# Kernel optimization log

Hardware: AMD Instinct MI355X
Metric: run time of the kernel (lower is better)

## Reference

```python
import jax, jax.numpy as jnp
import numpy as np


def _conv3x3(x, w, b):
    # NCHW conv, stride 1, pad 1
    y = jax.lax.conv_general_dilated(x, w, (1, 1), ((1, 1), (1, 1)),
                                     dimension_numbers=('NCHW', 'OIHW', 'NCHW'))
    return y + b[None, :, None, None]


def _deform_conv3x3(x, offset, w):
    # Deformable conv v1: 3x3, stride 1, pad 1, 1 deformable group, no bias.
    # offset: [B, 18, H, W] laid out as (dy_k, dx_k) for k = 0..8 (row-major taps).
    B, C, H, W = x.shape
    K = 9
    off = offset.reshape(B, K, 2, H, W)
    ky, kx = jnp.meshgrid(jnp.arange(3), jnp.arange(3), indexing='ij')
    ky = (ky.reshape(K) - 1).astype(x.dtype)  # kernel tap y-offset, pad=1
    kx = (kx.reshape(K) - 1).astype(x.dtype)
    hh = jnp.arange(H, dtype=x.dtype)
    ww = jnp.arange(W, dtype=x.dtype)
    # sampling locations [B, K, H, W]
    sy = hh[None, None, :, None] + ky[None, :, None, None] + off[:, :, 0]
    sx = ww[None, None, None, :] + kx[None, :, None, None] + off[:, :, 1]
    y0 = jnp.floor(sy)
    x0 = jnp.floor(sx)
    ly = sy - y0  # fractional parts
    lx = sx - x0
    x_flat = x.reshape(B, C, H * W)

    def gather(yi, xi, wgt):
        # zero-padding semantics: corners outside the image contribute 0
        valid = (yi >= 0) & (yi < H) & (xi >= 0) & (xi < W)
        idx = (jnp.clip(yi, 0, H - 1).astype(jnp.int32) * W
               + jnp.clip(xi, 0, W - 1).astype(jnp.int32)).reshape(B, 1, K * H * W)
        v = jnp.take_along_axis(x_flat, idx, axis=2).reshape(B, C, K, H, W)
        return v * (wgt * valid.astype(x.dtype))[:, None]

    sampled = (gather(y0,     x0,     (1 - ly) * (1 - lx))
             + gather(y0,     x0 + 1, (1 - ly) * lx)
             + gather(y0 + 1, x0,     ly * (1 - lx))
             + gather(y0 + 1, x0 + 1, ly * lx))  # [B, C, K, H, W]
    return jnp.einsum('bckhw,ock->bohw', sampled, w.reshape(w.shape[0], C, K))


def setup_inputs() -> dict:
    key = jax.random.key(0)
    ks = jax.random.split(key, 8)
    C, O = 256, 256
    return {
        'kernel': jax.random.normal(ks[0], (16, C, 16, 16), jnp.float32),
        'search': jax.random.normal(ks[1], (16, C, 32, 32), jnp.float32),
        'Toffset_w': jax.random.normal(ks[2], (18, C, 3, 3), jnp.float32) * 0.02,
        'Toffset_b': jnp.zeros((18,), jnp.float32),
        'Tdeform_w': jax.random.normal(ks[3], (O, C, 3, 3), jnp.float32) * 0.02,
        'Soffset_w': jax.random.normal(ks[4], (18, C, 3, 3), jnp.float32) * 0.02,
        'Soffset_b': jnp.zeros((18,), jnp.float32),
        'Sdeform_w': jax.random.normal(ks[5], (O, C, 3, 3), jnp.float32) * 0.02,
    }


def reference(kernel, search, Toffset_w, Toffset_b, Tdeform_w,
              Soffset_w, Soffset_b, Sdeform_w):
    kernel_offset = _conv3x3(kernel, Toffset_w, Toffset_b)
    kernel_out = _deform_conv3x3(kernel, kernel_offset, Tdeform_w)
    search_offset = _conv3x3(search, Soffset_w, Soffset_b)
    search_out = _deform_conv3x3(search, search_offset, Sdeform_w)
    return (kernel_out, search_out, kernel_offset, search_offset)
```

## Files before the change

### kernel.cpp

```cpp
#include <hip/hip_runtime.h>

#define CIN   256
#define OC    256
#define K_TOT 2304
#define CCH   32
#define NCHK  8
#define KCH   288
#define SSTR  296
#define DM    64
#define DUNITS (DM * 9 * 4)

#define N_DW  (OC * K_TOT)
#define N_OW  (32 * K_TOT)
#define N_CVT (2 * N_DW + 2 * N_OW)
#define CVT_BLOCKS (N_CVT / 4 / 256)

typedef short  bf16x8 __attribute__((ext_vector_type(8)));
typedef float  f32x4  __attribute__((ext_vector_type(4)));
typedef unsigned short ushort_t;

__device__ __forceinline__ ushort_t f2bf(float f) {
    unsigned u = __builtin_bit_cast(unsigned, f);
    u += 0x7fffu + ((u >> 16) & 1u);
    return (ushort_t)(u >> 16);
}
__device__ __forceinline__ float bf2f(short s) {
    return __builtin_bit_cast(float, ((unsigned)(unsigned short)s) << 16);
}

__global__ __launch_bounds__(256) void prep_k(
    const float* __restrict__ tdw, const float* __restrict__ sdw,
    const float* __restrict__ tow, const float* __restrict__ sow,
    const float* __restrict__ kin, const float* __restrict__ sin_,
    ushort_t* __restrict__ wk_d, ushort_t* __restrict__ ws_d,
    ushort_t* __restrict__ wk_o, ushort_t* __restrict__ ws_o,
    ushort_t* __restrict__ xt_k, ushort_t* __restrict__ xt_s)
{
    __shared__ ushort_t tile[64][264];

    if (blockIdx.x < CVT_BLOCKS) {
        const int i = (blockIdx.x * 256 + threadIdx.x) * 4;
        const float* src; ushort_t* dst; int j; bool offw = false;
        if (i < N_DW)                    { src = tdw; dst = wk_d; j = i; }
        else if (i < 2 * N_DW)           { src = sdw; dst = ws_d; j = i - N_DW; }
        else if (i < 2 * N_DW + N_OW)    { src = tow; dst = wk_o; j = i - 2 * N_DW; offw = true; }
        else                             { src = sow; dst = ws_o; j = i - 2 * N_DW - N_OW; offw = true; }
        const int oc = j / K_TOT;
        const int k  = j - oc * K_TOT;
        const int cc = k / KCH;
        const int r  = k - cc * KCH;
        const int tap = r >> 5;
        const int cl  = r & 31;
        ushort4 o4 = {0, 0, 0, 0};
        if (!offw || oc < 18) {
            const float* sp = &src[((size_t)oc * CIN + cc * 32 + cl) * 9 + tap];
            o4.x = f2bf(sp[0]); o4.y = f2bf(sp[9]); o4.z = f2bf(sp[18]); o4.w = f2bf(sp[27]);
        }
        *(ushort4*)&dst[j] = o4;
        return;
    }

    const int bx2 = blockIdx.x - CVT_BLOCKS;
    int H, W, b, px0; const float* x; ushort_t* xt;
    if (bx2 < 64) {
        H = 16; W = 16; x = kin; xt = xt_k;
        b = bx2 >> 2; px0 = (bx2 & 3) * 64;
    } else {
        int t2 = bx2 - 64;
        H = 32; W = 32; x = sin_; xt = xt_s;
        b = t2 >> 4; px0 = (t2 & 15) * 64;
    }
    const int HW = H * W;
    const int t = threadIdx.x, lane = t & 63, wv = t >> 6;
    const float* xb = x + (size_t)b * CIN * HW;

    for (int it = 0; it < 16; ++it) {
        const int ch = wv * 64 + it * 4 + (lane >> 4);
        const int pq = (lane & 15) * 4;
        float4 v = *(const float4*)&xb[(size_t)ch * HW + px0 + pq];
        tile[pq + 0][ch] = f2bf(v.x);
        tile[pq + 1][ch] = f2bf(v.y);
        tile[pq + 2][ch] = f2bf(v.z);
        tile[pq + 3][ch] = f2bf(v.w);
    }
    __syncthreads();
    for (int it = 0; it < 8; ++it) {
        const int px = it * 8 + wv * 2 + (lane >> 5);
        const int cg = (lane & 31) * 8;
        bf16x8 v = *(const bf16x8*)&tile[px][cg];
        *(bf16x8*)&xt[((size_t)b * HW + px0 + px) * 256 + cg] = v;
    }
}

__global__ __launch_bounds__(256, 2) void conv_gemm_k(
    const ushort_t* __restrict__ xt_k, const ushort_t* __restrict__ kwgt,
    const float* __restrict__ kbias, float* __restrict__ kout,
    const ushort_t* __restrict__ xt_s, const ushort_t* __restrict__ swgt,
    const float* __restrict__ sbias, float* __restrict__ sout)
{
    __shared__ float sred[3][4][2][64][4];

    int H, W, sh, b, px0;
    const ushort_t* xt; const ushort_t* wgt; const float* bias; float* out;
    if (blockIdx.x < 64) {
        H = 16; W = 16; sh = 4; xt = xt_k; wgt = kwgt; bias = kbias; out = kout;
        b = blockIdx.x >> 2; px0 = (blockIdx.x & 3) * 64;
    } else {
        int t2 = blockIdx.x - 64;
        H = 32; W = 32; sh = 5; xt = xt_s; wgt = swgt; bias = sbias; out = sout;
        b = t2 >> 4; px0 = (t2 & 15) * 64;
    }
    const int HW = H * W;
    const int t = threadIdx.x, lane = t & 63, kh = t >> 6;
    const int l15 = lane & 15;
    const int cg8 = (lane >> 4) * 8;
    const ushort_t* xtb = xt + (size_t)b * HW * 256;

    int h[4], wc[4];
#pragma unroll
    for (int mt = 0; mt < 4; ++mt) {
        const int px = px0 + mt * 16 + l15;
        h[mt]  = px >> sh;
        wc[mt] = px & (W - 1);
    }
    const ushort_t* wrow0 = wgt + (size_t)(l15)      * K_TOT + cg8;
    const ushort_t* wrow1 = wgt + (size_t)(16 + l15) * K_TOT + cg8;

    f32x4 acc[4][2] = {};
    for (int cc = kh * 2; cc < kh * 2 + 2; ++cc) {
        const int cb = cc * 32 + cg8;
#pragma unroll
        for (int ks = 0; ks < 9; ++ks) {
            const bf16x8 b0 = *(const bf16x8*)&wrow0[(size_t)cc * KCH + ks * 32];
            const bf16x8 b1 = *(const bf16x8*)&wrow1[(size_t)cc * KCH + ks * 32];
            const int dy = ks / 3 - 1, dx = ks % 3 - 1;
#pragma unroll
            for (int mt = 0; mt < 4; ++mt) {
                const int y  = h[mt] + dy;
                const int xx = wc[mt] + dx;
                const bool ok = ((unsigned)y < (unsigned)H) && ((unsigned)xx < (unsigned)W);
                bf16x8 a = {};
                if (ok) a = *(const bf16x8*)&xtb[(size_t)(((y << sh) + xx) * 256 + cb)];
                acc[mt][0] = __builtin_amdgcn_mfma_f32_16x16x32_bf16(a, b0, acc[mt][0], 0, 0, 0);
                acc[mt][1] = __builtin_amdgcn_mfma_f32_16x16x32_bf16(a, b1, acc[mt][1], 0, 0, 0);
            }
        }
    }

    if (kh > 0) {
#pragma unroll
        for (int mt = 0; mt < 4; ++mt)
#pragma unroll
            for (int nt = 0; nt < 2; ++nt)
                *(float4*)&sred[kh - 1][mt][nt][lane][0] = *(float4*)&acc[mt][nt];
    }
    __syncthreads();
    if (kh == 0) {
        const int prow = (lane >> 4) * 4;
#pragma unroll
        for (int nt = 0; nt < 2; ++nt) {
            const int oc = nt * 16 + l15;
            if (oc < 18) {
                const float bs = bias[oc];
#pragma unroll
                for (int mt = 0; mt < 4; ++mt) {
                    float4 r = *(float4*)&acc[mt][nt];
#pragma unroll
                    for (int q = 0; q < 3; ++q) {
                        const float4 o = *(const float4*)&sred[q][mt][nt][lane][0];
                        r.x += o.x; r.y += o.y; r.z += o.z; r.w += o.w;
                    }
                    r.x += bs; r.y += bs; r.z += bs; r.w += bs;
                    *(float4*)(out + ((size_t)b * 18 + oc) * HW + px0 + mt * 16 + prow) = r;
                }
            }
        }
    }
}

__device__ __forceinline__ void dcn_load4(
    bf16x8* c, const ushort_t* __restrict__ xtb, int4 id, int cb)
{
    c[0] = *(const bf16x8*)&xtb[(size_t)id.x * 256 + cb];
    c[1] = *(const bf16x8*)&xtb[(size_t)id.y * 256 + cb];
    c[2] = *(const bf16x8*)&xtb[(size_t)id.z * 256 + cb];
    c[3] = *(const bf16x8*)&xtb[(size_t)id.w * 256 + cb];
}
__device__ __forceinline__ void dcn_proc2(
    ushort_t* swb, int so, const bf16x8* c, float4 wt)
{
    bf16x8 r;
#pragma unroll
    for (int j = 0; j < 8; ++j) {
        const float v = wt.x * bf2f(c[0][j]) + wt.y * bf2f(c[1][j])
                      + wt.z * bf2f(c[2][j]) + wt.w * bf2f(c[3][j]);
        r[j] = (short)f2bf(v);
    }
    *(bf16x8*)&swb[so] = r;
}

__global__ __launch_bounds__(512, 4) void deform_gemm_k(
    const ushort_t* __restrict__ xt_k, const float* __restrict__ koffs,
    const ushort_t* __restrict__ kwgt, float* __restrict__ kout,
    const ushort_t* __restrict__ xt_s, const float* __restrict__ soffs,
    const ushort_t* __restrict__ swgt_, float* __restrict__ sout)
{
    __shared__ __align__(16) ushort_t smp[DM][SSTR];
    __shared__ __align__(16) int      sidx[DM][9][4];
    __shared__ __align__(16) float    swt [DM][9][4];

    int H, W, b, px0;
    const ushort_t* xt; const float* offs; const ushort_t* wgt; float* out;
    if (blockIdx.x < 64) {
        H = 16; W = 16; xt = xt_k; offs = koffs; wgt = kwgt; out = kout;
        b = blockIdx.x >> 2; px0 = (blockIdx.x & 3) * 64;
    } else {
        int t2 = blockIdx.x - 64;
        H = 32; W = 32; xt = xt_s; offs = soffs; wgt = swgt_; out = sout;
        b = t2 >> 4; px0 = (t2 & 15) * 64;
    }
    const int HW = H * W;
    const int t = threadIdx.x, lane = t & 63, wv = t >> 6;

#pragma unroll
    for (int u = 0; u < 2; ++u) {
        const int s = t + u * 512;
        if (s < DM * 9) {
            const int p = s / 9, k = s - 9 * p;
            const int pix = px0 + p;
            const int h  = pix / W;
            const int wc = pix - h * W;
            const float* ob = offs + (size_t)b * 18 * HW;
            const float dy = ob[(2 * k    ) * HW + pix];
            const float dx = ob[(2 * k + 1) * HW + pix];
            const float sy = (float)(h  + k / 3 - 1) + dy;
            const float sx = (float)(wc + k % 3 - 1) + dx;
            const float y0f = floorf(sy), x0f = floorf(sx);
            const float ly = sy - y0f, lx = sx - x0f;
            const int y0 = (int)y0f, x0 = (int)x0f;
#pragma unroll
            for (int j = 0; j < 4; ++j) {
                const int yy = y0 + (j >> 1);
                const int xx = x0 + (j & 1);
                const bool ok = ((unsigned)yy < (unsigned)H) && ((unsigned)xx < (unsigned)W);
                sidx[p][k][j] = min(max(yy, 0), H - 1) * W + min(max(xx, 0), W - 1);
                const float wj = ((j >> 1) ? ly : 1.f - ly) * ((j & 1) ? lx : 1.f - lx);
                swt[p][k][j] = ok ? wj : 0.f;
            }
        }
    }
    __syncthreads();

    const ushort_t* xtb = xt + (size_t)b * HW * 256;
    const int l15 = lane & 15;
    const int cg8 = (lane >> 4) * 8;
    const int ocb = wv * 32;
    const bool live4 = (t < 256);

    const int g0  = t >> 2;
    const int cgE = (t & 3) * 8;
    int uso[5];
#pragma unroll
    for (int q = 0; q < 5; ++q) {
        const int g  = g0 + q * 128;
        const int px = g / 9, tap = g - 9 * px;
        uso[q] = px * SSTR + tap * 32 + (t & 3) * 8;
    }

    const ushort_t* wrow0 = wgt + (size_t)(ocb      + l15) * K_TOT + cg8;
    const ushort_t* wrow1 = wgt + (size_t)(ocb + 16 + l15) * K_TOT + cg8;
    ushort_t* smpb = &smp[0][0];
    const int4*   sidxF = (const int4*)  &sidx[0][0][0];
    const float4* swtF  = (const float4*)&swt [0][0][0];

    f32x4 acc[4][2] = {};

    for (int cc = 0; cc < NCHK; ++cc) {
        const int cb = cc * 32 + cgE;
        const size_t kg0 = (size_t)cc * KCH;

#pragma unroll
        for (int q = 0; q < 5; ++q) {
            if (q < 4 || live4) {
                const int  g  = g0 + q * 128;
                const int4   id = sidxF[g];
                const float4 wt = swtF[g];
                bf16x8 c[4];
                dcn_load4(c, xtb, id, cb);
                dcn_proc2(smpb, uso[q], c, wt);
            }
        }

        const bf16x8 pb0 = *(const bf16x8*)&wrow0[kg0];
        const bf16x8 pb1 = *(const bf16x8*)&wrow1[kg0];

        asm volatile("s_waitcnt lgkmcnt(0)" ::: "memory");
        __builtin_amdgcn_sched_barrier(0);
        __builtin_amdgcn_s_barrier();
        __builtin_amdgcn_sched_barrier(0);

        __builtin_amdgcn_s_setprio(1);
#pragma unroll
        for (int ks = 0; ks < 9; ++ks) {
            const bf16x8 b0 = (ks == 0) ? pb0 : *(const bf16x8*)&wrow0[kg0 + (size_t)ks * 32];
            const bf16x8 b1 = (ks == 0) ? pb1 : *(const bf16x8*)&wrow1[kg0 + (size_t)ks * 32];
            bf16x8 a[4];
#pragma unroll
            for (int mt = 0; mt < 4; ++mt)
                a[mt] = *(const bf16x8*)&smp[mt * 16 + l15][ks * 32 + cg8];
#pragma unroll
            for (int mt = 0; mt < 4; ++mt) {
                acc[mt][0] = __builtin_amdgcn_mfma_f32_16x16x32_bf16(a[mt], b0, acc[mt][0], 0, 0, 0);
                acc[mt][1] = __builtin_amdgcn_mfma_f32_16x16x32_bf16(a[mt], b1, acc[mt][1], 0, 0, 0);
            }
        }
        __builtin_amdgcn_s_setprio(0);

        if (cc < NCHK - 1) {
            __builtin_amdgcn_sched_barrier(0);
            __builtin_amdgcn_s_barrier();
            __builtin_amdgcn_sched_barrier(0);
        }
    }

    const int prow = (lane >> 4) * 4;
#pragma unroll
    for (int mt = 0; mt < 4; ++mt) {
#pragma unroll
        for (int nt = 0; nt < 2; ++nt) {
            const int oc = ocb + nt * 16 + l15;
            float* op = out + ((size_t)b * OC + oc) * HW + px0 + mt * 16 + prow;
            *(float4*)op = *(float4*)&acc[mt][nt];
        }
    }
}

extern "C" void kernel_launch(void* const* d_in, const int* in_sizes, int n_in,
                              void* d_out, int out_size, void* d_ws, size_t ws_size,
                              hipStream_t stream) {
    const float* kin = (const float*)d_in[0];
    const float* sin_ = (const float*)d_in[1];
    const float* tow = (const float*)d_in[2];
    const float* tob = (const float*)d_in[3];
    const float* tdw = (const float*)d_in[4];
    const float* sow = (const float*)d_in[5];
    const float* sob = (const float*)d_in[6];
    const float* sdw = (const float*)d_in[7];

    float* out = (float*)d_out;
    float* out_k  = out;
    float* out_s  = out_k + (size_t)16 * 256 * 16 * 16;
    float* out_ko = out_s + (size_t)16 * 256 * 32 * 32;
    float* out_so = out_ko + (size_t)16 * 18 * 16 * 16;

    ushort_t* wk_d = (ushort_t*)d_ws;
    ushort_t* ws_d = wk_d + N_DW;
    ushort_t* wk_o = ws_d + N_DW;
    ushort_t* ws_o = wk_o + N_OW;
    ushort_t* xt_k = ws_o + N_OW;
    ushort_t* xt_s = xt_k + (size_t)16 * 256 * 256;

    prep_k<<<dim3(CVT_BLOCKS + 320), 256, 0, stream>>>(
        tdw, sdw, tow, sow, kin, sin_,
        wk_d, ws_d, wk_o, ws_o, xt_k, xt_s);

    conv_gemm_k<<<dim3(320), 256, 0, stream>>>(
        xt_k, wk_o, tob, out_ko, xt_s, ws_o, sob, out_so);

    deform_gemm_k<<<dim3(320), 512, 0, stream>>>(
        xt_k, out_ko, wk_d, out_k, xt_s, out_so, ws_d, out_s);
}
```

Measured before the change: 207.7 us.

## Software-pipeline deformable gathers and weight loads, remap blocks across XCDs

Restructures the deform-GEMM main loop so bilinear corner gathers for several tap groups are issued before earlier groups are processed. The first group for the next channel chunk is prefetched before the MFMA phase, so gather latency overlaps the matrix math. Weight fragments are double-buffered across the ks loop, and block indices are remapped so consecutive blocks (which go to different XCDs) handle different batches. This adds register pressure from holding five gather sets, which could cut occupancy under the 512x4 launch bounds.

```diff
diff --git a/kernel.cpp b/kernel.cpp
--- a/kernel.cpp
+++ b/kernel.cpp
@@ -8,7 +8,6 @@
 #define KCH   288
 #define SSTR  296
 #define DM    64
-#define DUNITS (DM * 9 * 4)
 
 #define N_DW  (OC * K_TOT)
 #define N_OW  (32 * K_TOT)
@@ -212,12 +211,14 @@
     int H, W, b, px0;
     const ushort_t* xt; const float* offs; const ushort_t* wgt; float* out;
     if (blockIdx.x < 64) {
+        const int xcd = blockIdx.x & 7, i = blockIdx.x >> 3;
         H = 16; W = 16; xt = xt_k; offs = koffs; wgt = kwgt; out = kout;
-        b = blockIdx.x >> 2; px0 = (blockIdx.x & 3) * 64;
+        b = xcd + 8 * (i & 1); px0 = (i >> 1) * 64;
     } else {
-        int t2 = blockIdx.x - 64;
+        const int t2 = blockIdx.x - 64;
+        const int xcd = t2 & 7, i = t2 >> 3;
         H = 32; W = 32; xt = xt_s; offs = soffs; wgt = swgt_; out = sout;
-        b = t2 >> 4; px0 = (t2 & 15) * 64;
+        b = xcd + 8 * (i & 1); px0 = (i >> 1) * 64;
     }
     const int HW = H * W;
     const int t = threadIdx.x, lane = t & 63, wv = t >> 6;
@@ -274,25 +275,38 @@
     const float4* swtF  = (const float4*)&swt [0][0][0];
 
     f32x4 acc[4][2] = {};
+    bf16x8 c0[4], c1[4], c2[4], c3[4], c4[4];
+    float4 w0v, w1v, w2v, w3v, w4v = {};
+    bf16x8 bq[2][2];
+
+    {
+        const int4 id = sidxF[g0];
+        w0v = swtF[g0];
+        dcn_load4(c0, xtb, id, cgE);
+    }
 
     for (int cc = 0; cc < NCHK; ++cc) {
         const int cb = cc * 32 + cgE;
         const size_t kg0 = (size_t)cc * KCH;
 
-#pragma unroll
-        for (int q = 0; q < 5; ++q) {
-            if (q < 4 || live4) {
-                const int  g  = g0 + q * 128;
-                const int4   id = sidxF[g];
-                const float4 wt = swtF[g];
-                bf16x8 c[4];
-                dcn_load4(c, xtb, id, cb);
-                dcn_proc2(smpb, uso[q], c, wt);
-            }
-        }
-
-        const bf16x8 pb0 = *(const bf16x8*)&wrow0[kg0];
-        const bf16x8 pb1 = *(const bf16x8*)&wrow1[kg0];
+        { const int4 id = sidxF[g0 + 128]; w1v = swtF[g0 + 128]; dcn_load4(c1, xtb, id, cb); }
+        { const int4 id = sidxF[g0 + 256]; w2v = swtF[g0 + 256]; dcn_load4(c2, xtb, id, cb); }
+        bq[0][0] = *(const bf16x8*)&wrow0[kg0];
+        bq[0][1] = *(const bf16x8*)&wrow1[kg0];
+
+        dcn_proc2(smpb, uso[0], c0, w0v);
+        { const int4 id = sidxF[g0 + 384]; w3v = swtF[g0 + 384]; dcn_load4(c3, xtb, id, cb); }
+        dcn_proc2(smpb, uso[1], c1, w1v);
+        if (live4) { const int4 id = sidxF[g0 + 512]; w4v = swtF[g0 + 512]; dcn_load4(c4, xtb, id, cb); }
+        dcn_proc2(smpb, uso[2], c2, w2v);
+        dcn_proc2(smpb, uso[3], c3, w3v);
+        if (live4) dcn_proc2(smpb, uso[4], c4, w4v);
+
+        if (cc < NCHK - 1) {
+            const int4 id = sidxF[g0];
+            w0v = swtF[g0];
+            dcn_load4(c0, xtb, id, cb + 32);
+        }
 
         asm volatile("s_waitcnt lgkmcnt(0)" ::: "memory");
         __builtin_amdgcn_sched_barrier(0);
@@ -302,16 +316,18 @@
         __builtin_amdgcn_s_setprio(1);
 #pragma unroll
         for (int ks = 0; ks < 9; ++ks) {
-            const bf16x8 b0 = (ks == 0) ? pb0 : *(const bf16x8*)&wrow0[kg0 + (size_t)ks * 32];
-            const bf16x8 b1 = (ks == 0) ? pb1 : *(const bf16x8*)&wrow1[kg0 + (size_t)ks * 32];
+            if (ks < 8) {
+                bq[(ks + 1) & 1][0] = *(const bf16x8*)&wrow0[kg0 + (size_t)(ks + 1) * 32];
+                bq[(ks + 1) & 1][1] = *(const bf16x8*)&wrow1[kg0 + (size_t)(ks + 1) * 32];
+            }
             bf16x8 a[4];
 #pragma unroll
             for (int mt = 0; mt < 4; ++mt)
                 a[mt] = *(const bf16x8*)&smp[mt * 16 + l15][ks * 32 + cg8];
 #pragma unroll
             for (int mt = 0; mt < 4; ++mt) {
-                acc[mt][0] = __builtin_amdgcn_mfma_f32_16x16x32_bf16(a[mt], b0, acc[mt][0], 0, 0, 0);
-                acc[mt][1] = __builtin_amdgcn_mfma_f32_16x16x32_bf16(a[mt], b1, acc[mt][1], 0, 0, 0);
+                acc[mt][0] = __builtin_amdgcn_mfma_f32_16x16x32_bf16(a[mt], bq[ks & 1][0], acc[mt][0], 0, 0, 0);
+                acc[mt][1] = __builtin_amdgcn_mfma_f32_16x16x32_bf16(a[mt], bq[ks & 1][1], acc[mt][1], 0, 0, 0);
             }
         }
         __builtin_amdgcn_s_setprio(0);
```

After: 265.6 us. 1.28x slower.

## Warp-specialize deform GEMM into producer/consumer waves with double-buffered samples

Applied to the files above, without the earlier changes.

Splits the deformable-conv GEMM block into four producer waves that bilinearly sample into a double-buffered LDS tile and four consumer waves that run MFMA with register-prefetched, nontemporal weight loads. The pixel tile shrinks from 64 to 32, so twice as many blocks launch, and blocks are remapped so batches spread across XCDs. The goal is to overlap gather latency with matrix math and raise parallelism. In exchange, each block now reads the weights for half as many pixels, which doubles total weight traffic. Half the waves also do no MFMA work.

```diff
diff --git a/kernel.cpp b/kernel.cpp
--- a/kernel.cpp
+++ b/kernel.cpp
@@ -7,8 +7,7 @@
 #define NCHK  8
 #define KCH   288
 #define SSTR  296
-#define DM    64
-#define DUNITS (DM * 9 * 4)
+#define DM    32
 
 #define N_DW  (OC * K_TOT)
 #define N_OW  (32 * K_TOT)
@@ -26,6 +25,9 @@
 }
 __device__ __forceinline__ float bf2f(short s) {
     return __builtin_bit_cast(float, ((unsigned)(unsigned short)s) << 16);
+}
+__device__ __forceinline__ bf16x8 ldnt(const ushort_t* p) {
+    return __builtin_nontemporal_load((const bf16x8*)p);
 }
 
 __global__ __launch_bounds__(256) void prep_k(
@@ -205,48 +207,46 @@
     const ushort_t* __restrict__ xt_s, const float* __restrict__ soffs,
     const ushort_t* __restrict__ swgt_, float* __restrict__ sout)
 {
-    __shared__ __align__(16) ushort_t smp[DM][SSTR];
+    __shared__ __align__(16) ushort_t smp[2][DM][SSTR];
     __shared__ __align__(16) int      sidx[DM][9][4];
     __shared__ __align__(16) float    swt [DM][9][4];
 
     int H, W, b, px0;
     const ushort_t* xt; const float* offs; const ushort_t* wgt; float* out;
-    if (blockIdx.x < 64) {
+    if (blockIdx.x < 128) {
+        const int xcd = blockIdx.x & 7, i = blockIdx.x >> 3;
         H = 16; W = 16; xt = xt_k; offs = koffs; wgt = kwgt; out = kout;
-        b = blockIdx.x >> 2; px0 = (blockIdx.x & 3) * 64;
+        b = xcd + 8 * (i & 1); px0 = (i >> 1) * 32;
     } else {
-        int t2 = blockIdx.x - 64;
+        const int t2 = blockIdx.x - 128;
+        const int xcd = t2 & 7, i = t2 >> 3;
         H = 32; W = 32; xt = xt_s; offs = soffs; wgt = swgt_; out = sout;
-        b = t2 >> 4; px0 = (t2 & 15) * 64;
+        b = xcd + 8 * (i & 1); px0 = (i >> 1) * 32;
     }
     const int HW = H * W;
     const int t = threadIdx.x, lane = t & 63, wv = t >> 6;
 
-#pragma unroll
-    for (int u = 0; u < 2; ++u) {
-        const int s = t + u * 512;
-        if (s < DM * 9) {
-            const int p = s / 9, k = s - 9 * p;
-            const int pix = px0 + p;
-            const int h  = pix / W;
-            const int wc = pix - h * W;
-            const float* ob = offs + (size_t)b * 18 * HW;
-            const float dy = ob[(2 * k    ) * HW + pix];
-            const float dx = ob[(2 * k + 1) * HW + pix];
-            const float sy = (float)(h  + k / 3 - 1) + dy;
-            const float sx = (float)(wc + k % 3 - 1) + dx;
-            const float y0f = floorf(sy), x0f = floorf(sx);
-            const float ly = sy - y0f, lx = sx - x0f;
-            const int y0 = (int)y0f, x0 = (int)x0f;
-#pragma unroll
-            for (int j = 0; j < 4; ++j) {
-                const int yy = y0 + (j >> 1);
-                const int xx = x0 + (j & 1);
-                const bool ok = ((unsigned)yy < (unsigned)H) && ((unsigned)xx < (unsigned)W);
-                sidx[p][k][j] = min(max(yy, 0), H - 1) * W + min(max(xx, 0), W - 1);
-                const float wj = ((j >> 1) ? ly : 1.f - ly) * ((j & 1) ? lx : 1.f - lx);
-                swt[p][k][j] = ok ? wj : 0.f;
-            }
+    if (t < DM * 9) {
+        const int p = t / 9, k = t - 9 * p;
+        const int pix = px0 + p;
+        const int h  = pix / W;
+        const int wc = pix - h * W;
+        const float* ob = offs + (size_t)b * 18 * HW;
+        const float dy = ob[(2 * k    ) * HW + pix];
+        const float dx = ob[(2 * k + 1) * HW + pix];
+        const float sy = (float)(h  + k / 3 - 1) + dy;
+        const float sx = (float)(wc + k % 3 - 1) + dx;
+        const float y0f = floorf(sy), x0f = floorf(sx);
+        const float ly = sy - y0f, lx = sx - x0f;
+        const int y0 = (int)y0f, x0 = (int)x0f;
+#pragma unroll
+        for (int j = 0; j < 4; ++j) {
+            const int yy = y0 + (j >> 1);
+            const int xx = x0 + (j & 1);
+            const bool ok = ((unsigned)yy < (unsigned)H) && ((unsigned)xx < (unsigned)W);
+            sidx[p][k][j] = min(max(yy, 0), H - 1) * W + min(max(xx, 0), W - 1);
+            const float wj = ((j >> 1) ? ly : 1.f - ly) * ((j & 1) ? lx : 1.f - lx);
+            swt[p][k][j] = ok ? wj : 0.f;
         }
     }
     __syncthreads();
@@ -254,64 +254,87 @@
     const ushort_t* xtb = xt + (size_t)b * HW * 256;
     const int l15 = lane & 15;
     const int cg8 = (lane >> 4) * 8;
-    const int ocb = wv * 32;
-    const bool live4 = (t < 256);
-
-    const int g0  = t >> 2;
-    const int cgE = (t & 3) * 8;
-    int uso[5];
-#pragma unroll
-    for (int q = 0; q < 5; ++q) {
-        const int g  = g0 + q * 128;
-        const int px = g / 9, tap = g - 9 * px;
-        uso[q] = px * SSTR + tap * 32 + (t & 3) * 8;
-    }
-
-    const ushort_t* wrow0 = wgt + (size_t)(ocb      + l15) * K_TOT + cg8;
-    const ushort_t* wrow1 = wgt + (size_t)(ocb + 16 + l15) * K_TOT + cg8;
-    ushort_t* smpb = &smp[0][0];
-    const int4*   sidxF = (const int4*)  &sidx[0][0][0];
-    const float4* swtF  = (const float4*)&swt [0][0][0];
-
-    f32x4 acc[4][2] = {};
+
+    if (wv < 4) {
+        const int g0  = t >> 2;
+        const int cgE = (t & 3) * 8;
+        const bool live4 = (t < 128);
+        int uso[5];
+#pragma unroll
+        for (int q = 0; q < 5; ++q) {
+            const int g  = g0 + q * 64;
+            const int px = g / 9, tap = g - 9 * px;
+            uso[q] = px * SSTR + tap * 32 + (t & 3) * 8;
+        }
+        const int4*   sidxF = (const int4*)  &sidx[0][0][0];
+        const float4* swtF  = (const float4*)&swt [0][0][0];
+
+        for (int cp = 0; cp < NCHK; ++cp) {
+            ushort_t* swb = &smp[cp & 1][0][0];
+            const int cb = cp * 32 + cgE;
+
+            bf16x8 cA[4], cB[4], cC[4];
+            float4 wA, wB, wC;
+            { const int4 id = sidxF[g0];       wA = swtF[g0];       dcn_load4(cA, xtb, id, cb); }
+            { const int4 id = sidxF[g0 + 64];  wB = swtF[g0 + 64];  dcn_load4(cB, xtb, id, cb); }
+            { const int4 id = sidxF[g0 + 128]; wC = swtF[g0 + 128]; dcn_load4(cC, xtb, id, cb); }
+            dcn_proc2(swb, uso[0], cA, wA);
+            { const int4 id = sidxF[g0 + 192]; wA = swtF[g0 + 192]; dcn_load4(cA, xtb, id, cb); }
+            dcn_proc2(swb, uso[1], cB, wB);
+            if (live4) { const int4 id = sidxF[g0 + 256]; wB = swtF[g0 + 256]; dcn_load4(cB, xtb, id, cb); }
+            dcn_proc2(swb, uso[2], cC, wC);
+            dcn_proc2(swb, uso[3], cA, wA);
+            if (live4) dcn_proc2(swb, uso[4], cB, wB);
+
+            asm volatile("s_waitcnt lgkmcnt(0)" ::: "memory");
+            __builtin_amdgcn_sched_barrier(0);
+            __builtin_amdgcn_s_barrier();
+            __builtin_amdgcn_sched_barrier(0);
+        }
+        return;
+    }
+
+    const int w = wv - 4;
+    const ushort_t* wr0 = wgt + (size_t)(w * 64 +  0 + l15) * K_TOT + cg8;
+    const ushort_t* wr1 = wgt + (size_t)(w * 64 + 16 + l15) * K_TOT + cg8;
+    const ushort_t* wr2 = wgt + (size_t)(w * 64 + 32 + l15) * K_TOT + cg8;
+    const ushort_t* wr3 = wgt + (size_t)(w * 64 + 48 + l15) * K_TOT + cg8;
+
+    f32x4 acc[2][4] = {};
+    bf16x8 bq[3][4];
+    bq[0][0] = ldnt(&wr0[0]);  bq[0][1] = ldnt(&wr1[0]);
+    bq[0][2] = ldnt(&wr2[0]);  bq[0][3] = ldnt(&wr3[0]);
+    bq[1][0] = ldnt(&wr0[32]); bq[1][1] = ldnt(&wr1[32]);
+    bq[1][2] = ldnt(&wr2[32]); bq[1][3] = ldnt(&wr3[32]);
+
+    __builtin_amdgcn_sched_barrier(0);
+    __builtin_amdgcn_s_barrier();
+    __builtin_amdgcn_sched_barrier(0);
 
     for (int cc = 0; cc < NCHK; ++cc) {
-        const int cb = cc * 32 + cgE;
+        const ushort_t (*sw)[SSTR] = smp[cc & 1];
         const size_t kg0 = (size_t)cc * KCH;
 
-#pragma unroll
-        for (int q = 0; q < 5; ++q) {
-            if (q < 4 || live4) {
-                const int  g  = g0 + q * 128;
-                const int4   id = sidxF[g];
-                const float4 wt = swtF[g];
-                bf16x8 c[4];
-                dcn_load4(c, xtb, id, cb);
-                dcn_proc2(smpb, uso[q], c, wt);
+        __builtin_amdgcn_s_setprio(1);
+#pragma unroll
+        for (int ks = 0; ks < 9; ++ks) {
+            const int ls = (ks + 2) % 3;
+            if (cc < NCHK - 1 || ks < 7) {
+                const size_t kgl = (ks < 7)
+                    ? kg0 + (size_t)(ks + 2) * 32
+                    : kg0 + KCH + (size_t)(ks - 7) * 32;
+                bq[ls][0] = ldnt(&wr0[kgl]);
+                bq[ls][1] = ldnt(&wr1[kgl]);
+                bq[ls][2] = ldnt(&wr2[kgl]);
+                bq[ls][3] = ldnt(&wr3[kgl]);
             }
-        }
-
-        const bf16x8 pb0 = *(const bf16x8*)&wrow0[kg0];
-        const bf16x8 pb1 = *(const bf16x8*)&wrow1[kg0];
-
-        asm volatile("s_waitcnt lgkmcnt(0)" ::: "memory");
-        __builtin_amdgcn_sched_barrier(0);
-        __builtin_amdgcn_s_barrier();
-        __builtin_amdgcn_sched_barrier(0);
-
-        __builtin_amdgcn_s_setprio(1);
-#pragma unroll
-        for (int ks = 0; ks < 9; ++ks) {
-            const bf16x8 b0 = (ks == 0) ? pb0 : *(const bf16x8*)&wrow0[kg0 + (size_t)ks * 32];
-            const bf16x8 b1 = (ks == 0) ? pb1 : *(const bf16x8*)&wrow1[kg0 + (size_t)ks * 32];
-            bf16x8 a[4];
-#pragma unroll
-            for (int mt = 0; mt < 4; ++mt)
-                a[mt] = *(const bf16x8*)&smp[mt * 16 + l15][ks * 32 + cg8];
-#pragma unroll
-            for (int mt = 0; mt < 4; ++mt) {
-                acc[mt][0] = __builtin_amdgcn_mfma_f32_16x16x32_bf16(a[mt], b0, acc[mt][0], 0, 0, 0);
-                acc[mt][1] = __builtin_amdgcn_mfma_f32_16x16x32_bf16(a[mt], b1, acc[mt][1], 0, 0, 0);
+            const bf16x8 a0 = *(const bf16x8*)&sw[l15     ][ks * 32 + cg8];
+            const bf16x8 a1 = *(const bf16x8*)&sw[16 + l15][ks * 32 + cg8];
+            const int cs = ks % 3;
+#pragma unroll
+            for (int nt = 0; nt < 4; ++nt) {
+                acc[0][nt] = __builtin_amdgcn_mfma_f32_16x16x32_bf16(a0, bq[cs][nt], acc[0][nt], 0, 0, 0);
+                acc[1][nt] = __builtin_amdgcn_mfma_f32_16x16x32_bf16(a1, bq[cs][nt], acc[1][nt], 0, 0, 0);
             }
         }
         __builtin_amdgcn_s_setprio(0);
@@ -325,10 +348,10 @@
 
     const int prow = (lane >> 4) * 4;
 #pragma unroll
-    for (int mt = 0; mt < 4; ++mt) {
-#pragma unroll
-        for (int nt = 0; nt < 2; ++nt) {
-            const int oc = ocb + nt * 16 + l15;
+    for (int mt = 0; mt < 2; ++mt) {
+#pragma unroll
+        for (int nt = 0; nt < 4; ++nt) {
+            const int oc = w * 64 + nt * 16 + l15;
             float* op = out + ((size_t)b * OC + oc) * HW + px0 + mt * 16 + prow;
             *(float4*)op = *(float4*)&acc[mt][nt];
         }
@@ -367,6 +390,6 @@
     conv_gemm_k<<<dim3(320), 256, 0, stream>>>(
         xt_k, wk_o, tob, out_ko, xt_s, ws_o, sob, out_so);
 
-    deform_gemm_k<<<dim3(320), 512, 0, stream>>>(
+    deform_gemm_k<<<dim3(640), 512, 0, stream>>>(
         xt_k, out_ko, wk_d, out_k, xt_s, out_so, ws_d, out_s);
 }
```

After: 304.0 us. 46.4% more time.
